# Performance work log

Measured on AMD Instinct MI355X. Metric: run time of the kernel, lower is better.

The kernel has to match this reference:

```python
import jax, jax.numpy as jnp
import numpy as np

N_NODES = 50000
N_EDGES = 800000
IN_C = 128
HID = 128
OUT_C = 64
N_GRAPHS = 256


def setup_inputs() -> dict:
    key = jax.random.key(0)
    ks = jax.random.split(key, 12)
    x = jax.random.normal(ks[0], (N_NODES, IN_C), dtype=jnp.float32)
    edge_index = jax.random.randint(ks[1], (2, N_EDGES), 0, N_NODES, dtype=jnp.int32)
    batch = jnp.sort(jax.random.randint(ks[2], (N_NODES,), 0, N_GRAPHS, dtype=jnp.int32))
    def lin(k, fan_in, fan_out):
        bound = 1.0 / np.sqrt(fan_in)
        kw, kb = jax.random.split(k)
        W = jax.random.uniform(kw, (fan_in, fan_out), minval=-bound, maxval=bound, dtype=jnp.float32)
        b = jax.random.uniform(kb, (fan_out,), minval=-bound, maxval=bound, dtype=jnp.float32)
        return W, b
    W1a, b1a = lin(ks[3], IN_C, HID)
    W1b, b1b = lin(ks[4], HID, HID)
    W2a, b2a = lin(ks[5], HID, HID)
    W2b, b2b = lin(ks[6], HID, HID)
    Wl, bl = lin(ks[7], HID, OUT_C)
    return {"x": x, "edge_index": edge_index, "batch": batch,
            "W1a": W1a, "b1a": b1a, "W1b": W1b, "b1b": b1b,
            "W2a": W2a, "b2a": b2a, "W2b": W2b, "b2b": b2b,
            "Wl": Wl, "bl": bl}


def gin_conv(x, edge_index, Wa, ba, Wb, bb):
    # GINConv with eps=0: h_i = MLP(x_i + sum_{j->i} x_j)
    src, dst = edge_index[0], edge_index[1]
    agg = jax.ops.segment_sum(x[src], dst, num_segments=x.shape[0])  # [N, d]
    h = x + agg
    h = jax.nn.relu(h @ Wa + ba) @ Wb + bb
    return h


def reference(x, edge_index, batch, W1a, b1a, W1b, b1b, W2a, b2a, W2b, b2b, Wl, bl):
    h = gin_conv(x, edge_index, W1a, b1a, W1b, b1b)
    h = gin_conv(h, edge_index, W2a, b2a, W2b, b2b)
    # global mean pool over graphs in the batch
    sums = jax.ops.segment_sum(h, batch, num_segments=N_GRAPHS)          # [G, HID]
    cnts = jax.ops.segment_sum(jnp.ones((h.shape[0],), h.dtype), batch, num_segments=N_GRAPHS)
    pooled = sums / jnp.maximum(cnts, 1.0)[:, None]
    return pooled @ Wl + bl  # [G, OUT_C]
```

## Files before the change

### kernel.cpp

```cpp
#include <hip/hip_runtime.h>

constexpr int N  = 50000;
constexpr int E  = 800000;
constexpr int C  = 128;
constexpr int G  = 256;
constexpr int OC = 64;
constexpr int D  = 64;

constexpr int NBUCK = 196;
constexpr int BCAP  = 5120;
constexpr int EPB = 2048;
constexpr int EB = (E + EPB - 1) / EPB;
constexpr int WB = 256;
constexpr int XB = (N * C / 8 + 255) / 256;
constexpr int GB = (N + 255) / 256;

typedef __attribute__((ext_vector_type(8))) short short8;
typedef __attribute__((ext_vector_type(4))) float f32x4;
typedef __attribute__((ext_vector_type(2))) float f32x2;

__device__ __forceinline__ unsigned int au(float f) { return __float_as_uint(f); }

__device__ __forceinline__ unsigned short f2bf(float f) {
    unsigned int u = au(f);
    u += 0x7fffu + ((u >> 16) & 1u);
    return (unsigned short)(u >> 16);
}
__device__ __forceinline__ unsigned int pack_bf16(float lo, float hi) {
    return ((au(hi) + 0x8000u) & 0xFFFF0000u) | ((au(lo) + 0x8000u) >> 16);
}

__device__ __forceinline__ void acc16(f32x2* a, uint4 v) {
    a[0] += __builtin_amdgcn_cvt_pk_f32_fp8((int)v.x, false);
    a[1] += __builtin_amdgcn_cvt_pk_f32_fp8((int)v.x, true);
    a[2] += __builtin_amdgcn_cvt_pk_f32_fp8((int)v.y, false);
    a[3] += __builtin_amdgcn_cvt_pk_f32_fp8((int)v.y, true);
    a[4] += __builtin_amdgcn_cvt_pk_f32_fp8((int)v.z, false);
    a[5] += __builtin_amdgcn_cvt_pk_f32_fp8((int)v.z, true);
    a[6] += __builtin_amdgcn_cvt_pk_f32_fp8((int)v.w, false);
    a[7] += __builtin_amdgcn_cvt_pk_f32_fp8((int)v.w, true);
}
__device__ __forceinline__ void set16(f32x2* a, uint4 v) {
    a[0] = __builtin_amdgcn_cvt_pk_f32_fp8((int)v.x, false);
    a[1] = __builtin_amdgcn_cvt_pk_f32_fp8((int)v.x, true);
    a[2] = __builtin_amdgcn_cvt_pk_f32_fp8((int)v.y, false);
    a[3] = __builtin_amdgcn_cvt_pk_f32_fp8((int)v.y, true);
    a[4] = __builtin_amdgcn_cvt_pk_f32_fp8((int)v.z, false);
    a[5] = __builtin_amdgcn_cvt_pk_f32_fp8((int)v.z, true);
    a[6] = __builtin_amdgcn_cvt_pk_f32_fp8((int)v.w, false);
    a[7] = __builtin_amdgcn_cvt_pk_f32_fp8((int)v.w, true);
}


__global__ __launch_bounds__(256) void build_prep_kernel(const int* __restrict__ src,
                                                         const int* __restrict__ dst,
                                                         int* __restrict__ bcount,
                                                         unsigned int* __restrict__ bucketbuf,
                                                         const float* __restrict__ W1a,
                                                         const float* __restrict__ W1b,
                                                         const float* __restrict__ W2a,
                                                         const float* __restrict__ W2b,
                                                         const float* __restrict__ x,
                                                         unsigned short* __restrict__ wt,
                                                         unsigned int* __restrict__ x8,
                                                         const int* __restrict__ batch,
                                                         int* __restrict__ gcnt) {
    int b = blockIdx.x;
    if (b < EB) {
        __shared__ int lcount[NBUCK];
        __shared__ int lbase[NBUCK];
        __shared__ int lcur[NBUCK];
        int tid = threadIdx.x;
        for (int i = tid; i < NBUCK; i += 256) { lcount[i] = 0; lcur[i] = 0; }
        __syncthreads();
        int e0 = b * EPB;
        int sv[8], dv[8];
#pragma unroll
        for (int i = 0; i < 8; ++i) {
            int e = e0 + i * 256 + tid;
            if (e < E) {
                sv[i] = src[e];
                dv[i] = dst[e];
                atomicAdd(&lcount[dv[i] >> 8], 1);
            } else {
                dv[i] = -1;
            }
        }
        __syncthreads();
        if (tid < NBUCK) {
            int c = lcount[tid];
            lbase[tid] = (c > 0) ? atomicAdd(&bcount[tid], c) : 0;
        }
        __syncthreads();
#pragma unroll
        for (int i = 0; i < 8; ++i) {
            if (dv[i] >= 0) {
                int bk = dv[i] >> 8;
                int pos = lbase[bk] + atomicAdd(&lcur[bk], 1);
                if (pos < BCAP)
                    bucketbuf[(size_t)bk * BCAP + pos] =
                        ((unsigned int)sv[i] << 16) | (unsigned int)(dv[i] & 255);
            }
        }
    } else if (b < EB + WB) {
        const float* Ws[4] = {W1a, W1b, W2a, W2b};
        int idx = (b - EB) * 256 + threadIdx.x;
        int which = idx >> 14;
        int el    = idx & 16383;
        int n = el >> 7, k = el & 127;
        wt[idx] = f2bf(Ws[which][k * 128 + n]);
    } else if (b < EB + WB + XB) {
        int idx = (b - EB - WB) * 256 + threadIdx.x;
        const float4* x4 = (const float4*)x;
        float4 v0 = x4[idx * 2];
        float4 v1 = x4[idx * 2 + 1];
        unsigned int lo = 0, hi = 0;
        lo = (unsigned int)__builtin_amdgcn_cvt_pk_fp8_f32(v0.x, v0.y, (int)lo, false);
        lo = (unsigned int)__builtin_amdgcn_cvt_pk_fp8_f32(v0.z, v0.w, (int)lo, true);
        hi = (unsigned int)__builtin_amdgcn_cvt_pk_fp8_f32(v1.x, v1.y, (int)hi, false);
        hi = (unsigned int)__builtin_amdgcn_cvt_pk_fp8_f32(v1.z, v1.w, (int)hi, true);
        ((uint2*)x8)[idx] = make_uint2(lo, hi);
    } else {
        __shared__ int h[G];
        int tid = threadIdx.x;
        h[tid] = 0;
        __syncthreads();
        int i = (b - EB - WB - XB) * 256 + tid;
        if (i < N) atomicAdd(&h[batch[i]], 1);
        __syncthreads();
        int c = h[tid];
        if (c > 0) atomicAdd(&gcnt[tid], c);
    }
}


__global__ __launch_bounds__(256) void bucket_fill_kernel(const int* __restrict__ bcount,
                                                          const unsigned int* __restrict__ bucketbuf,
                                                          unsigned short* __restrict__ ell,
                                                          int* __restrict__ deg) {
    __shared__ int lcur[256];
    int b = blockIdx.x;
    int tid = threadIdx.x;
    lcur[tid] = 0;
    __syncthreads();
    int cnt = min(bcount[b], BCAP);
    const unsigned int* buf = bucketbuf + (size_t)b * BCAP;
    int nbase = b << 8;
    for (int i = tid; i < cnt; i += 256) {
        unsigned int e = buf[i];
        int dlow = (int)(e & 255u);
        int p = atomicAdd(&lcur[dlow], 1);
        if (p < D) ell[(size_t)(nbase + dlow) * D + p] = (unsigned short)(e >> 16);
    }
    __syncthreads();
    int node = nbase + tid;
    if (node < N) deg[node] = lcur[tid];
}


__global__ __launch_bounds__(512, 6) void conv_kernel(const unsigned char* __restrict__ Fg,
                                                      const int* __restrict__ deg,
                                                      const unsigned short* __restrict__ ell,
                                                      const unsigned short* __restrict__ WaT,
                                                      const float* __restrict__ ba,
                                                      const unsigned short* __restrict__ WbT,
                                                      const float* __restrict__ bb,
                                                      unsigned char* __restrict__ Hg8,
                                                      const int* __restrict__ batch,
                                                      float* __restrict__ gsum,
                                                      int outFp8) {
    constexpr int LD = 136;
    __shared__ short Xl[64 * LD];
    __shared__ short Wl[128 * LD];
    int tid  = threadIdx.x;
    int lane = tid & 63;
    int wave = tid >> 6;
    int row0 = blockIdx.x * 64;

    const short8* Wa8 = (const short8*)WaT;
#pragma unroll
    for (int i = tid; i < 2048; i += 512) {
        int r = i >> 4, c = i & 15;
        *((short8*)(Wl + r * LD) + c) = Wa8[i];
    }

    {
        int grp = tid >> 3;
        int l   = tid & 7;
        const uint4* F16 = (const uint4*)Fg;
        int n = row0 + grp;
        f32x2 a[8];
        if (n < N) {
            int dg = min(deg[n], D);
            const uint4* irow = (const uint4*)(ell + (size_t)n * D);
            set16(a, F16[(size_t)n * 8 + l]);
            int nb  = dg >> 3;
            int rem = dg & 7;
            if (nb > 0) {
                uint4 i4 = irow[0];
                int t0 = (int)(i4.x & 0xffffu), t1 = (int)(i4.x >> 16);
                int t2 = (int)(i4.y & 0xffffu), t3 = (int)(i4.y >> 16);
                int t4 = (int)(i4.z & 0xffffu), t5 = (int)(i4.z >> 16);
                int t6 = (int)(i4.w & 0xffffu), t7 = (int)(i4.w >> 16);
                uint4 v0 = F16[(size_t)t0 * 8 + l];
                uint4 v1 = F16[(size_t)t1 * 8 + l];
                uint4 v2 = F16[(size_t)t2 * 8 + l];
                uint4 v3 = F16[(size_t)t3 * 8 + l];
                uint4 v4 = F16[(size_t)t4 * 8 + l];
                uint4 v5 = F16[(size_t)t5 * 8 + l];
                uint4 v6 = F16[(size_t)t6 * 8 + l];
                uint4 v7 = F16[(size_t)t7 * 8 + l];
                for (int b = 1; b < nb; ++b) {
                    uint4 j4 = irow[b];
                    int u0 = (int)(j4.x & 0xffffu), u1 = (int)(j4.x >> 16);
                    int u2 = (int)(j4.y & 0xffffu), u3 = (int)(j4.y >> 16);
                    int u4 = (int)(j4.z & 0xffffu), u5 = (int)(j4.z >> 16);
                    int u6 = (int)(j4.w & 0xffffu), u7 = (int)(j4.w >> 16);
                    uint4 w0 = F16[(size_t)u0 * 8 + l];
                    uint4 w1 = F16[(size_t)u1 * 8 + l];
                    uint4 w2 = F16[(size_t)u2 * 8 + l];
                    uint4 w3 = F16[(size_t)u3 * 8 + l];
                    uint4 w4 = F16[(size_t)u4 * 8 + l];
                    uint4 w5 = F16[(size_t)u5 * 8 + l];
                    uint4 w6 = F16[(size_t)u6 * 8 + l];
                    uint4 w7 = F16[(size_t)u7 * 8 + l];
                    acc16(a, v0); acc16(a, v1); acc16(a, v2); acc16(a, v3);
                    acc16(a, v4); acc16(a, v5); acc16(a, v6); acc16(a, v7);
                    v0 = w0; v1 = w1; v2 = w2; v3 = w3;
                    v4 = w4; v5 = w5; v6 = w6; v7 = w7;
                }
                acc16(a, v0); acc16(a, v1); acc16(a, v2); acc16(a, v3);
                acc16(a, v4); acc16(a, v5); acc16(a, v6); acc16(a, v7);
            }
            if (rem) {
                uint4 i4 = irow[nb];
                int t0 = (int)(i4.x & 0xffffu), t1 = (int)(i4.x >> 16);
                int t2 = (int)(i4.y & 0xffffu), t3 = (int)(i4.y >> 16);
                int t4 = (int)(i4.z & 0xffffu), t5 = (int)(i4.z >> 16);
                int t6 = (int)(i4.w & 0xffffu), t7 = (int)(i4.w >> 16);
                int tv[8] = {t0, t1, t2, t3, t4, t5, t6, t7};
#pragma unroll
                for (int m = 0; m < 7; ++m) {
                    if (m < rem) {
                        uint4 v = F16[(size_t)tv[m] * 8 + l];
                        acc16(a, v);
                    }
                }
            }
        } else {
#pragma unroll
            for (int q = 0; q < 8; ++q) a[q] = (f32x2){0.f, 0.f};
        }
        uint4 o0, o1;
        o0.x = pack_bf16(a[0].x, a[0].y); o0.y = pack_bf16(a[1].x, a[1].y);
        o0.z = pack_bf16(a[2].x, a[2].y); o0.w = pack_bf16(a[3].x, a[3].y);
        o1.x = pack_bf16(a[4].x, a[4].y); o1.y = pack_bf16(a[5].x, a[5].y);
        o1.z = pack_bf16(a[6].x, a[6].y); o1.w = pack_bf16(a[7].x, a[7].y);
        uint4* xp = (uint4*)(Xl + grp * LD + l * 16);
        xp[0] = o0;
        xp[1] = o1;
    }

    int mw = wave >> 2, nw = wave & 3;
    int lid = lane & 15, quad = lane >> 4;

    f32x4 acc[2][2];
#pragma unroll
    for (int nt = 0; nt < 2; ++nt) {
        float b = ba[nw * 32 + nt * 16 + lid];
        acc[0][nt] = (f32x4){b, b, b, b};
        acc[1][nt] = (f32x4){b, b, b, b};
    }
    __syncthreads();

#pragma unroll
    for (int ks = 0; ks < 4; ++ks) {
        short8 a0 = *(const short8*)(Xl + (mw * 32 + lid) * LD + ks * 32 + quad * 8);
        short8 a1 = *(const short8*)(Xl + (mw * 32 + 16 + lid) * LD + ks * 32 + quad * 8);
#pragma unroll
        for (int nt = 0; nt < 2; ++nt) {
            short8 bf = *(const short8*)(Wl + (nw * 32 + nt * 16 + lid) * LD + ks * 32 + quad * 8);
            acc[0][nt] = __builtin_amdgcn_mfma_f32_16x16x32_bf16(a0, bf, acc[0][nt], 0, 0, 0);
            acc[1][nt] = __builtin_amdgcn_mfma_f32_16x16x32_bf16(a1, bf, acc[1][nt], 0, 0, 0);
        }
    }
    __syncthreads();

#pragma unroll
    for (int mt = 0; mt < 2; ++mt) {
#pragma unroll
        for (int nt = 0; nt < 2; ++nt) {
            int mbase = mw * 32 + mt * 16 + quad * 4;
            int n = nw * 32 + nt * 16 + lid;
            f32x4 v = acc[mt][nt];
#pragma unroll
            for (int r = 0; r < 4; ++r)
                Xl[(mbase + r) * LD + n] = (short)f2bf(fmaxf(v[r], 0.f));
        }
    }
    const short8* Wb8 = (const short8*)WbT;
#pragma unroll
    for (int i = tid; i < 2048; i += 512) {
        int r = i >> 4, c = i & 15;
        *((short8*)(Wl + r * LD) + c) = Wb8[i];
    }
    f32x4 acc2[2][2];
#pragma unroll
    for (int nt = 0; nt < 2; ++nt) {
        float b = bb[nw * 32 + nt * 16 + lid];
        acc2[0][nt] = (f32x4){b, b, b, b};
        acc2[1][nt] = (f32x4){b, b, b, b};
    }
    __syncthreads();

#pragma unroll
    for (int ks = 0; ks < 4; ++ks) {
        short8 a0 = *(const short8*)(Xl + (mw * 32 + lid) * LD + ks * 32 + quad * 8);
        short8 a1 = *(const short8*)(Xl + (mw * 32 + 16 + lid) * LD + ks * 32 + quad * 8);
#pragma unroll
        for (int nt = 0; nt < 2; ++nt) {
            short8 bf = *(const short8*)(Wl + (nw * 32 + nt * 16 + lid) * LD + ks * 32 + quad * 8);
            acc2[0][nt] = __builtin_amdgcn_mfma_f32_16x16x32_bf16(a0, bf, acc2[0][nt], 0, 0, 0);
            acc2[1][nt] = __builtin_amdgcn_mfma_f32_16x16x32_bf16(a1, bf, acc2[1][nt], 0, 0, 0);
        }
    }

#pragma unroll
    for (int mt = 0; mt < 2; ++mt) {
#pragma unroll
        for (int nt = 0; nt < 2; ++nt) {
            int mbase = row0 + mw * 32 + mt * 16 + quad * 4;
            int n = nw * 32 + nt * 16 + lid;
            f32x4 v = acc2[mt][nt];
            if (outFp8) {
#pragma unroll
                for (int r = 0; r < 4; ++r) {
                    int row = mbase + r;
                    if (row < N) {
                        unsigned int p = (unsigned int)__builtin_amdgcn_cvt_pk_fp8_f32(v[r], 0.f, 0, false);
                        Hg8[(size_t)row * 128 + n] = (unsigned char)(p & 0xFF);
                    }
                }
            } else {
                int gprev = -1;
                float s = 0.f;
#pragma unroll
                for (int r = 0; r < 4; ++r) {
                    int row = mbase + r;
                    if (row < N) {
                        int g = batch[row];
                        if (g != gprev) {
                            if (gprev >= 0) atomicAdd(&gsum[gprev * C + n], s);
                            gprev = g;
                            s = 0.f;
                        }
                        s += v[r];
                    }
                }
                if (gprev >= 0) atomicAdd(&gsum[gprev * C + n], s);
            }
        }
    }
}


__global__ __launch_bounds__(64) void head_kernel(const float* __restrict__ gsum,
                                                  const int* __restrict__ gcnt,
                                                  const float* __restrict__ Wl,
                                                  const float* __restrict__ bl,
                                                  float* __restrict__ out) {
    int g = blockIdx.x;
    int t = threadIdx.x;
    __shared__ float pooled[C];
    float inv = 1.0f / (float)max(gcnt[g], 1);
    pooled[t]      = gsum[g * C + t] * inv;
    pooled[t + 64] = gsum[g * C + 64 + t] * inv;
    __syncthreads();
    float o = bl[t];
#pragma unroll 4
    for (int k = 0; k < C; ++k) o += pooled[k] * Wl[k * OC + t];
    out[g * OC + t] = o;
}


extern "C" void kernel_launch(void* const* d_in, const int* in_sizes, int n_in,
                              void* d_out, int out_size, void* d_ws, size_t ws_size,
                              hipStream_t stream) {
    const float* x    = (const float*)d_in[0];
    const int*   ei   = (const int*)d_in[1];
    const int*   bat  = (const int*)d_in[2];
    const float* W1a  = (const float*)d_in[3];
    const float* b1a  = (const float*)d_in[4];
    const float* W1b  = (const float*)d_in[5];
    const float* b1b  = (const float*)d_in[6];
    const float* W2a  = (const float*)d_in[7];
    const float* b2a  = (const float*)d_in[8];
    const float* W2b  = (const float*)d_in[9];
    const float* b2b  = (const float*)d_in[10];
    const float* Wl   = (const float*)d_in[11];
    const float* bl   = (const float*)d_in[12];
    float*       out  = (float*)d_out;

    float* gsum    = (float*)d_ws;
    int*   gcnt    = (int*)(gsum + G * C);
    int*   bcount  = gcnt + G;
    int*   deg     = bcount + NBUCK;
    unsigned int* bucketbuf = (unsigned int*)(deg + N);
    unsigned short* ell = (unsigned short*)(bucketbuf + (size_t)NBUCK * BCAP);
    unsigned short* wt  = ell + (size_t)N * D;
    unsigned char*  x8  = (unsigned char*)(wt + 4 * 16384);
    unsigned char*  h8  = x8 + (size_t)N * 128;

    const unsigned short* wt1a = wt;
    const unsigned short* wt1b = wt + 16384;
    const unsigned short* wt2a = wt + 2 * 16384;
    const unsigned short* wt2b = wt + 3 * 16384;

    const int* src = ei;
    const int* dst = ei + E;

    hipMemsetAsync(gsum, 0, (size_t)(G * C + G + NBUCK) * sizeof(int), stream);

    build_prep_kernel<<<EB + WB + XB + GB, 256, 0, stream>>>(src, dst, bcount, bucketbuf,
                                                             W1a, W1b, W2a, W2b, x,
                                                             wt, (unsigned int*)x8,
                                                             bat, gcnt);
    bucket_fill_kernel<<<NBUCK, 256, 0, stream>>>(bcount, bucketbuf, ell, deg);

    int mb = (N + 63) / 64;

    conv_kernel<<<mb, 512, 0, stream>>>(x8, deg, ell, wt1a, b1a, wt1b, b1b,
                                        h8, nullptr, nullptr, 1);
    conv_kernel<<<mb, 512, 0, stream>>>(h8, deg, ell, wt2a, b2a, wt2b, b2b,
                                        nullptr, bat, gsum, 0);

    head_kernel<<<G, 64, 0, stream>>>(gsum, gcnt, Wl, bl, out);
}
```

Baseline: 214.2 us.

## Build ELL adjacency directly with global atomics, drop bucket pass

Replaces the two-stage bucketed CSR/ELL build (local bucket counting plus a separate bucket_fill kernel) with a single pass that does a global atomicAdd on each destination's degree and writes the source index straight into the ELL slot. This removes one kernel launch and the intermediate bucket buffer traffic, and the memset grows to zero the degree array. It also lowers the conv_kernel occupancy hint in launch_bounds from 6 to 4, which allows more registers per thread. The trade-off is 800k scattered global atomics on random nodes instead of mostly shared-memory atomics.

```diff
diff --git a/kernel.cpp b/kernel.cpp
--- a/kernel.cpp
+++ b/kernel.cpp
@@ -7,8 +7,6 @@
 constexpr int OC = 64;
 constexpr int D  = 64;
 
-constexpr int NBUCK = 196;
-constexpr int BCAP  = 5120;
 constexpr int EPB = 2048;
 constexpr int EB = (E + EPB - 1) / EPB;
 constexpr int WB = 256;
@@ -54,8 +52,8 @@
 
 __global__ __launch_bounds__(256) void build_prep_kernel(const int* __restrict__ src,
                                                          const int* __restrict__ dst,
-                                                         int* __restrict__ bcount,
-                                                         unsigned int* __restrict__ bucketbuf,
+                                                         int* __restrict__ deg,
+                                                         unsigned short* __restrict__ ell,
                                                          const float* __restrict__ W1a,
                                                          const float* __restrict__ W1b,
                                                          const float* __restrict__ W2a,
@@ -67,39 +65,16 @@
                                                          int* __restrict__ gcnt) {
     int b = blockIdx.x;
     if (b < EB) {
-        __shared__ int lcount[NBUCK];
-        __shared__ int lbase[NBUCK];
-        __shared__ int lcur[NBUCK];
+        int e0 = b * EPB;
         int tid = threadIdx.x;
-        for (int i = tid; i < NBUCK; i += 256) { lcount[i] = 0; lcur[i] = 0; }
-        __syncthreads();
-        int e0 = b * EPB;
-        int sv[8], dv[8];
 #pragma unroll
         for (int i = 0; i < 8; ++i) {
             int e = e0 + i * 256 + tid;
             if (e < E) {
-                sv[i] = src[e];
-                dv[i] = dst[e];
-                atomicAdd(&lcount[dv[i] >> 8], 1);
-            } else {
-                dv[i] = -1;
-            }
-        }
-        __syncthreads();
-        if (tid < NBUCK) {
-            int c = lcount[tid];
-            lbase[tid] = (c > 0) ? atomicAdd(&bcount[tid], c) : 0;
-        }
-        __syncthreads();
-#pragma unroll
-        for (int i = 0; i < 8; ++i) {
-            if (dv[i] >= 0) {
-                int bk = dv[i] >> 8;
-                int pos = lbase[bk] + atomicAdd(&lcur[bk], 1);
-                if (pos < BCAP)
-                    bucketbuf[(size_t)bk * BCAP + pos] =
-                        ((unsigned int)sv[i] << 16) | (unsigned int)(dv[i] & 255);
+                int s = src[e];
+                int d = dst[e];
+                int p = atomicAdd(&deg[d], 1);
+                if (p < D) ell[(size_t)d * D + p] = (unsigned short)s;
             }
         }
     } else if (b < EB + WB) {
@@ -134,31 +109,7 @@
 }
 
 
-__global__ __launch_bounds__(256) void bucket_fill_kernel(const int* __restrict__ bcount,
-                                                          const unsigned int* __restrict__ bucketbuf,
-                                                          unsigned short* __restrict__ ell,
-                                                          int* __restrict__ deg) {
-    __shared__ int lcur[256];
-    int b = blockIdx.x;
-    int tid = threadIdx.x;
-    lcur[tid] = 0;
-    __syncthreads();
-    int cnt = min(bcount[b], BCAP);
-    const unsigned int* buf = bucketbuf + (size_t)b * BCAP;
-    int nbase = b << 8;
-    for (int i = tid; i < cnt; i += 256) {
-        unsigned int e = buf[i];
-        int dlow = (int)(e & 255u);
-        int p = atomicAdd(&lcur[dlow], 1);
-        if (p < D) ell[(size_t)(nbase + dlow) * D + p] = (unsigned short)(e >> 16);
-    }
-    __syncthreads();
-    int node = nbase + tid;
-    if (node < N) deg[node] = lcur[tid];
-}
-
-
-__global__ __launch_bounds__(512, 6) void conv_kernel(const unsigned char* __restrict__ Fg,
+__global__ __launch_bounds__(512, 4) void conv_kernel(const unsigned char* __restrict__ Fg,
                                                       const int* __restrict__ deg,
                                                       const unsigned short* __restrict__ ell,
                                                       const unsigned short* __restrict__ WaT,
@@ -403,10 +354,8 @@
 
     float* gsum    = (float*)d_ws;
     int*   gcnt    = (int*)(gsum + G * C);
-    int*   bcount  = gcnt + G;
-    int*   deg     = bcount + NBUCK;
-    unsigned int* bucketbuf = (unsigned int*)(deg + N);
-    unsigned short* ell = (unsigned short*)(bucketbuf + (size_t)NBUCK * BCAP);
+    int*   deg     = gcnt + G;
+    unsigned short* ell = (unsigned short*)(deg + N);
     unsigned short* wt  = ell + (size_t)N * D;
     unsigned char*  x8  = (unsigned char*)(wt + 4 * 16384);
     unsigned char*  h8  = x8 + (size_t)N * 128;
@@ -419,13 +368,12 @@
     const int* src = ei;
     const int* dst = ei + E;
 
-    hipMemsetAsync(gsum, 0, (size_t)(G * C + G + NBUCK) * sizeof(int), stream);
-
-    build_prep_kernel<<<EB + WB + XB + GB, 256, 0, stream>>>(src, dst, bcount, bucketbuf,
+    hipMemsetAsync(gsum, 0, (size_t)(G * C + G + N) * sizeof(int), stream);
+
+    build_prep_kernel<<<EB + WB + XB + GB, 256, 0, stream>>>(src, dst, deg, ell,
                                                              W1a, W1b, W2a, W2b, x,
                                                              wt, (unsigned int*)x8,
                                                              bat, gcnt);
-    bucket_fill_kernel<<<NBUCK, 256, 0, stream>>>(bcount, bucketbuf, ell, deg);
 
     int mb = (N + 63) / 64;
 
```

Result: slower. 233.8 us (+9.2%).

## Reassociate GIN linear layers: transform before aggregation and fold consecutive weights

Applied to the files above, without the earlier changes.

Uses linearity of aggregation to apply W1a before the neighbor sum, folds W1b·W2a into a single precomputed matrix (and bias b1b into a degree-scaled term), and folds W2b into the head weights so the last conv needs only aggregation, ReLU and pooling. This removes two of the four per-node GEMMs and the x fp8 conversion pass. In exchange it adds a separate dense GEMM kernel before aggregation and quantizes pre-activation products to fp8, which changes numerics. The gather loop is also reduced from 8-wide to 4-wide index batches.

```diff
diff --git a/kernel.cpp b/kernel.cpp
--- a/kernel.cpp
+++ b/kernel.cpp
@@ -10,10 +10,11 @@
 constexpr int NBUCK = 196;
 constexpr int BCAP  = 5120;
 constexpr int EPB = 2048;
-constexpr int EB = (E + EPB - 1) / EPB;
-constexpr int WB = 256;
-constexpr int XB = (N * C / 8 + 255) / 256;
-constexpr int GB = (N + 255) / 256;
+constexpr int EB  = (E + EPB - 1) / EPB;
+constexpr int WB1 = 64;
+constexpr int WXB = 64;
+constexpr int WHB = 32;
+constexpr int GB  = (N + 255) / 256;
 
 typedef __attribute__((ext_vector_type(8))) short short8;
 typedef __attribute__((ext_vector_type(4))) float f32x4;
@@ -51,6 +52,44 @@
     a[7] = __builtin_amdgcn_cvt_pk_f32_fp8((int)v.w, true);
 }
 
+__device__ __forceinline__ void gather_rows(f32x2* a, const uint4* F16,
+                                            const unsigned short* irow, int dg, int l) {
+    const uint2* i2 = (const uint2*)irow;
+    int nb  = dg >> 2;
+    int rem = dg & 3;
+    if (nb > 0) {
+        uint2 iu = i2[0];
+        int t0 = (int)(iu.x & 0xffffu), t1 = (int)(iu.x >> 16);
+        int t2 = (int)(iu.y & 0xffffu), t3 = (int)(iu.y >> 16);
+        uint4 v0 = F16[(size_t)t0 * 8 + l];
+        uint4 v1 = F16[(size_t)t1 * 8 + l];
+        uint4 v2 = F16[(size_t)t2 * 8 + l];
+        uint4 v3 = F16[(size_t)t3 * 8 + l];
+        for (int b = 1; b < nb; ++b) {
+            uint2 ju = i2[b];
+            int u0 = (int)(ju.x & 0xffffu), u1 = (int)(ju.x >> 16);
+            int u2 = (int)(ju.y & 0xffffu), u3 = (int)(ju.y >> 16);
+            uint4 w0 = F16[(size_t)u0 * 8 + l];
+            uint4 w1 = F16[(size_t)u1 * 8 + l];
+            uint4 w2 = F16[(size_t)u2 * 8 + l];
+            uint4 w3 = F16[(size_t)u3 * 8 + l];
+            acc16(a, v0); acc16(a, v1); acc16(a, v2); acc16(a, v3);
+            v0 = w0; v1 = w1; v2 = w2; v3 = w3;
+        }
+        acc16(a, v0); acc16(a, v1); acc16(a, v2); acc16(a, v3);
+    }
+    if (rem) {
+        const unsigned short* ir = irow + nb * 4;
+#pragma unroll
+        for (int m = 0; m < 3; ++m) {
+            if (m < rem) {
+                uint4 v = F16[(size_t)ir[m] * 8 + l];
+                acc16(a, v);
+            }
+        }
+    }
+}
+
 
 __global__ __launch_bounds__(256) void build_prep_kernel(const int* __restrict__ src,
                                                          const int* __restrict__ dst,
@@ -60,17 +99,23 @@
                                                          const float* __restrict__ W1b,
                                                          const float* __restrict__ W2a,
                                                          const float* __restrict__ W2b,
-                                                         const float* __restrict__ x,
-                                                         unsigned short* __restrict__ wt,
-                                                         unsigned int* __restrict__ x8,
+                                                         const float* __restrict__ Wl,
+                                                         const float* __restrict__ bl,
+                                                         const float* __restrict__ b1b,
+                                                         const float* __restrict__ b2b,
+                                                         unsigned short* __restrict__ wt1a,
+                                                         unsigned short* __restrict__ wtx,
+                                                         float* __restrict__ Whead,
+                                                         float* __restrict__ c1,
+                                                         float* __restrict__ bhead,
                                                          const int* __restrict__ batch,
                                                          int* __restrict__ gcnt) {
     int b = blockIdx.x;
+    int tid = threadIdx.x;
     if (b < EB) {
         __shared__ int lcount[NBUCK];
         __shared__ int lbase[NBUCK];
         __shared__ int lcur[NBUCK];
-        int tid = threadIdx.x;
         for (int i = tid; i < NBUCK; i += 256) { lcount[i] = 0; lcur[i] = 0; }
         __syncthreads();
         int e0 = b * EPB;
@@ -102,30 +147,38 @@
                         ((unsigned int)sv[i] << 16) | (unsigned int)(dv[i] & 255);
             }
         }
-    } else if (b < EB + WB) {
-        const float* Ws[4] = {W1a, W1b, W2a, W2b};
-        int idx = (b - EB) * 256 + threadIdx.x;
-        int which = idx >> 14;
-        int el    = idx & 16383;
-        int n = el >> 7, k = el & 127;
-        wt[idx] = f2bf(Ws[which][k * 128 + n]);
-    } else if (b < EB + WB + XB) {
-        int idx = (b - EB - WB) * 256 + threadIdx.x;
-        const float4* x4 = (const float4*)x;
-        float4 v0 = x4[idx * 2];
-        float4 v1 = x4[idx * 2 + 1];
-        unsigned int lo = 0, hi = 0;
-        lo = (unsigned int)__builtin_amdgcn_cvt_pk_fp8_f32(v0.x, v0.y, (int)lo, false);
-        lo = (unsigned int)__builtin_amdgcn_cvt_pk_fp8_f32(v0.z, v0.w, (int)lo, true);
-        hi = (unsigned int)__builtin_amdgcn_cvt_pk_fp8_f32(v1.x, v1.y, (int)hi, false);
-        hi = (unsigned int)__builtin_amdgcn_cvt_pk_fp8_f32(v1.z, v1.w, (int)hi, true);
-        ((uint2*)x8)[idx] = make_uint2(lo, hi);
+    } else if (b < EB + WB1) {
+        int idx = (b - EB) * 256 + tid;
+        int n = idx >> 7, k = idx & 127;
+        wt1a[idx] = f2bf(W1a[k * 128 + n]);
+    } else if (b < EB + WB1 + WXB) {
+        int idx = (b - EB - WB1) * 256 + tid;
+        int i = idx >> 7, j = idx & 127;
+        float acc = 0.f;
+        for (int k = 0; k < 128; ++k) acc += W1b[i * 128 + k] * W2a[k * 128 + j];
+        wtx[j * 128 + i] = f2bf(acc);
+    } else if (b < EB + WB1 + WXB + WHB) {
+        int idx = (b - EB - WB1 - WXB) * 256 + tid;
+        int i = idx >> 6, j = idx & 63;
+        float acc = 0.f;
+        for (int k = 0; k < 128; ++k) acc += W2b[i * 128 + k] * Wl[k * OC + j];
+        Whead[i * OC + j] = acc;
+    } else if (b == EB + WB1 + WXB + WHB) {
+        if (tid < 128) {
+            float acc = 0.f;
+            for (int k = 0; k < 128; ++k) acc += b1b[k] * W2a[k * 128 + tid];
+            c1[tid] = acc;
+        } else if (tid < 192) {
+            int j = tid - 128;
+            float acc = bl[j];
+            for (int k = 0; k < 128; ++k) acc += b2b[k] * Wl[k * OC + j];
+            bhead[j] = acc;
+        }
     } else {
         __shared__ int h[G];
-        int tid = threadIdx.x;
         h[tid] = 0;
         __syncthreads();
-        int i = (b - EB - WB - XB) * 256 + tid;
+        int i = (b - (EB + WB1 + WXB + WHB + 1)) * 256 + tid;
         if (i < N) atomicAdd(&h[batch[i]], 1);
         __syncthreads();
         int c = h[tid];
@@ -158,94 +211,111 @@
 }
 
 
-__global__ __launch_bounds__(512, 6) void conv_kernel(const unsigned char* __restrict__ Fg,
-                                                      const int* __restrict__ deg,
-                                                      const unsigned short* __restrict__ ell,
-                                                      const unsigned short* __restrict__ WaT,
-                                                      const float* __restrict__ ba,
-                                                      const unsigned short* __restrict__ WbT,
-                                                      const float* __restrict__ bb,
-                                                      unsigned char* __restrict__ Hg8,
-                                                      const int* __restrict__ batch,
-                                                      float* __restrict__ gsum,
-                                                      int outFp8) {
+__global__ __launch_bounds__(256, 4) void gemma_kernel(const float* __restrict__ x,
+                                                       const unsigned short* __restrict__ wt1a,
+                                                       unsigned char* __restrict__ z1) {
     constexpr int LD = 136;
     __shared__ short Xl[64 * LD];
     __shared__ short Wl[128 * LD];
-    int tid  = threadIdx.x;
-    int lane = tid & 63;
-    int wave = tid >> 6;
+    int tid = threadIdx.x;
+    int lane = tid & 63, wave = tid >> 6;
     int row0 = blockIdx.x * 64;
 
-    const short8* Wa8 = (const short8*)WaT;
+    const short8* Wg = (const short8*)wt1a;
+#pragma unroll
+    for (int i = tid; i < 2048; i += 256) {
+        int r = i >> 4, c = i & 15;
+        *((short8*)(Wl + r * LD) + c) = Wg[i];
+    }
+    const float4* x4 = (const float4*)(x + (size_t)row0 * C);
+#pragma unroll
+    for (int i = tid; i < 2048; i += 256) {
+        int r = i >> 5, c4 = i & 31;
+        float4 v = (row0 + r < N) ? x4[i] : make_float4(0.f, 0.f, 0.f, 0.f);
+        uint2 u;
+        u.x = pack_bf16(v.x, v.y);
+        u.y = pack_bf16(v.z, v.w);
+        *(uint2*)(Xl + r * LD + c4 * 4) = u;
+    }
+
+    int mw = wave >> 1, nw = wave & 1;
+    int lid = lane & 15, quad = lane >> 4;
+    f32x4 acc[2][4];
+#pragma unroll
+    for (int nt = 0; nt < 4; ++nt) {
+        acc[0][nt] = (f32x4){0.f, 0.f, 0.f, 0.f};
+        acc[1][nt] = (f32x4){0.f, 0.f, 0.f, 0.f};
+    }
+    __syncthreads();
+
+#pragma unroll
+    for (int ks = 0; ks < 4; ++ks) {
+        short8 a0 = *(const short8*)(Xl + (mw * 32 + lid) * LD + ks * 32 + quad * 8);
+        short8 a1 = *(const short8*)(Xl + (mw * 32 + 16 + lid) * LD + ks * 32 + quad * 8);
+#pragma unroll
+        for (int nt = 0; nt < 4; ++nt) {
+            short8 bf = *(const short8*)(Wl + (nw * 64 + nt * 16 + lid) * LD + ks * 32 + quad * 8);
+            acc[0][nt] = __builtin_amdgcn_mfma_f32_16x16x32_bf16(a0, bf, acc[0][nt], 0, 0, 0);
+            acc[1][nt] = __builtin_amdgcn_mfma_f32_16x16x32_bf16(a1, bf, acc[1][nt], 0, 0, 0);
+        }
+    }
+
+#pragma unroll
+    for (int mt = 0; mt < 2; ++mt) {
+#pragma unroll
+        for (int nt = 0; nt < 4; ++nt) {
+            int mbase = row0 + mw * 32 + mt * 16 + quad * 4;
+            int n = nw * 64 + nt * 16 + lid;
+            f32x4 v = acc[mt][nt];
+#pragma unroll
+            for (int r = 0; r < 4; ++r) {
+                int row = mbase + r;
+                if (row < N) {
+                    unsigned int p = (unsigned int)__builtin_amdgcn_cvt_pk_fp8_f32(v[r], 0.f, 0, false);
+                    z1[(size_t)row * 128 + n] = (unsigned char)(p & 0xFF);
+                }
+            }
+        }
+    }
+}
+
+
+__global__ __launch_bounds__(512, 6) void k2_kernel(const unsigned char* __restrict__ z1,
+                                                    const int* __restrict__ deg,
+                                                    const unsigned short* __restrict__ ell,
+                                                    const unsigned short* __restrict__ wtx,
+                                                    const float* __restrict__ b1a,
+                                                    unsigned char* __restrict__ z2) {
+    constexpr int LD = 136;
+    __shared__ short Xl[64 * LD];
+    __shared__ short Wl[128 * LD];
+    int tid = threadIdx.x;
+    int lane = tid & 63, wave = tid >> 6;
+    int row0 = blockIdx.x * 64;
+
+    const short8* Wg = (const short8*)wtx;
 #pragma unroll
     for (int i = tid; i < 2048; i += 512) {
         int r = i >> 4, c = i & 15;
-        *((short8*)(Wl + r * LD) + c) = Wa8[i];
+        *((short8*)(Wl + r * LD) + c) = Wg[i];
     }
 
     {
         int grp = tid >> 3;
         int l   = tid & 7;
-        const uint4* F16 = (const uint4*)Fg;
+        const uint4* F16 = (const uint4*)z1;
         int n = row0 + grp;
         f32x2 a[8];
         if (n < N) {
-            int dg = min(deg[n], D);
-            const uint4* irow = (const uint4*)(ell + (size_t)n * D);
+            int dgc = min(deg[n], D);
             set16(a, F16[(size_t)n * 8 + l]);
-            int nb  = dg >> 3;
-            int rem = dg & 7;
-            if (nb > 0) {
-                uint4 i4 = irow[0];
-                int t0 = (int)(i4.x & 0xffffu), t1 = (int)(i4.x >> 16);
-                int t2 = (int)(i4.y & 0xffffu), t3 = (int)(i4.y >> 16);
-                int t4 = (int)(i4.z & 0xffffu), t5 = (int)(i4.z >> 16);
-                int t6 = (int)(i4.w & 0xffffu), t7 = (int)(i4.w >> 16);
-                uint4 v0 = F16[(size_t)t0 * 8 + l];
-                uint4 v1 = F16[(size_t)t1 * 8 + l];
-                uint4 v2 = F16[(size_t)t2 * 8 + l];
-                uint4 v3 = F16[(size_t)t3 * 8 + l];
-                uint4 v4 = F16[(size_t)t4 * 8 + l];
-                uint4 v5 = F16[(size_t)t5 * 8 + l];
-                uint4 v6 = F16[(size_t)t6 * 8 + l];
-                uint4 v7 = F16[(size_t)t7 * 8 + l];
-                for (int b = 1; b < nb; ++b) {
-                    uint4 j4 = irow[b];
-                    int u0 = (int)(j4.x & 0xffffu), u1 = (int)(j4.x >> 16);
-                    int u2 = (int)(j4.y & 0xffffu), u3 = (int)(j4.y >> 16);
-                    int u4 = (int)(j4.z & 0xffffu), u5 = (int)(j4.z >> 16);
-                    int u6 = (int)(j4.w & 0xffffu), u7 = (int)(j4.w >> 16);
-                    uint4 w0 = F16[(size_t)u0 * 8 + l];
-                    uint4 w1 = F16[(size_t)u1 * 8 + l];
-                    uint4 w2 = F16[(size_t)u2 * 8 + l];
-                    uint4 w3 = F16[(size_t)u3 * 8 + l];
-                    uint4 w4 = F16[(size_t)u4 * 8 + l];
-                    uint4 w5 = F16[(size_t)u5 * 8 + l];
-                    uint4 w6 = F16[(size_t)u6 * 8 + l];
-                    uint4 w7 = F16[(size_t)u7 * 8 + l];
-                    acc16(a, v0); acc16(a, v1); acc16(a, v2); acc16(a, v3);
-                    acc16(a, v4); acc16(a, v5); acc16(a, v6); acc16(a, v7);
-                    v0 = w0; v1 = w1; v2 = w2; v3 = w3;
-                    v4 = w4; v5 = w5; v6 = w6; v7 = w7;
-                }
-                acc16(a, v0); acc16(a, v1); acc16(a, v2); acc16(a, v3);
-                acc16(a, v4); acc16(a, v5); acc16(a, v6); acc16(a, v7);
-            }
-            if (rem) {
-                uint4 i4 = irow[nb];
-                int t0 = (int)(i4.x & 0xffffu), t1 = (int)(i4.x >> 16);
-                int t2 = (int)(i4.y & 0xffffu), t3 = (int)(i4.y >> 16);
-                int t4 = (int)(i4.z & 0xffffu), t5 = (int)(i4.z >> 16);
-                int t6 = (int)(i4.w & 0xffffu), t7 = (int)(i4.w >> 16);
-                int tv[8] = {t0, t1, t2, t3, t4, t5, t6, t7};
-#pragma unroll
-                for (int m = 0; m < 7; ++m) {
-                    if (m < rem) {
-                        uint4 v = F16[(size_t)tv[m] * 8 + l];
-                        acc16(a, v);
-                    }
-                }
+            gather_rows(a, F16, ell + (size_t)n * D, dgc, l);
+            const f32x2* bp = (const f32x2*)(b1a + l * 16);
+#pragma unroll
+            for (int q = 0; q < 8; ++q) {
+                a[q] += bp[q];
+                a[q].x = fmaxf(a[q].x, 0.f);
+                a[q].y = fmaxf(a[q].y, 0.f);
             }
         } else {
 #pragma unroll
@@ -263,13 +333,11 @@
 
     int mw = wave >> 2, nw = wave & 3;
     int lid = lane & 15, quad = lane >> 4;
-
     f32x4 acc[2][2];
 #pragma unroll
     for (int nt = 0; nt < 2; ++nt) {
-        float b = ba[nw * 32 + nt * 16 + lid];
-        acc[0][nt] = (f32x4){b, b, b, b};
-        acc[1][nt] = (f32x4){b, b, b, b};
+        acc[0][nt] = (f32x4){0.f, 0.f, 0.f, 0.f};
+        acc[1][nt] = (f32x4){0.f, 0.f, 0.f, 0.f};
     }
     __syncthreads();
 
@@ -284,46 +352,6 @@
             acc[1][nt] = __builtin_amdgcn_mfma_f32_16x16x32_bf16(a1, bf, acc[1][nt], 0, 0, 0);
         }
     }
-    __syncthreads();
-
-#pragma unroll
-    for (int mt = 0; mt < 2; ++mt) {
-#pragma unroll
-        for (int nt = 0; nt < 2; ++nt) {
-            int mbase = mw * 32 + mt * 16 + quad * 4;
-            int n = nw * 32 + nt * 16 + lid;
-            f32x4 v = acc[mt][nt];
-#pragma unroll
-            for (int r = 0; r < 4; ++r)
-                Xl[(mbase + r) * LD + n] = (short)f2bf(fmaxf(v[r], 0.f));
-        }
-    }
-    const short8* Wb8 = (const short8*)WbT;
-#pragma unroll
-    for (int i = tid; i < 2048; i += 512) {
-        int r = i >> 4, c = i & 15;
-        *((short8*)(Wl + r * LD) + c) = Wb8[i];
-    }
-    f32x4 acc2[2][2];
-#pragma unroll
-    for (int nt = 0; nt < 2; ++nt) {
-        float b = bb[nw * 32 + nt * 16 + lid];
-        acc2[0][nt] = (f32x4){b, b, b, b};
-        acc2[1][nt] = (f32x4){b, b, b, b};
-    }
-    __syncthreads();
-
-#pragma unroll
-    for (int ks = 0; ks < 4; ++ks) {
-        short8 a0 = *(const short8*)(Xl + (mw * 32 + lid) * LD + ks * 32 + quad * 8);
-        short8 a1 = *(const short8*)(Xl + (mw * 32 + 16 + lid) * LD + ks * 32 + quad * 8);
-#pragma unroll
-        for (int nt = 0; nt < 2; ++nt) {
-            short8 bf = *(const short8*)(Wl + (nw * 32 + nt * 16 + lid) * LD + ks * 32 + quad * 8);
-            acc2[0][nt] = __builtin_amdgcn_mfma_f32_16x16x32_bf16(a0, bf, acc2[0][nt], 0, 0, 0);
-            acc2[1][nt] = __builtin_amdgcn_mfma_f32_16x16x32_bf16(a1, bf, acc2[1][nt], 0, 0, 0);
-        }
-    }
 
 #pragma unroll
     for (int mt = 0; mt < 2; ++mt) {
@@ -331,43 +359,97 @@
         for (int nt = 0; nt < 2; ++nt) {
             int mbase = row0 + mw * 32 + mt * 16 + quad * 4;
             int n = nw * 32 + nt * 16 + lid;
-            f32x4 v = acc2[mt][nt];
-            if (outFp8) {
-#pragma unroll
-                for (int r = 0; r < 4; ++r) {
-                    int row = mbase + r;
-                    if (row < N) {
-                        unsigned int p = (unsigned int)__builtin_amdgcn_cvt_pk_fp8_f32(v[r], 0.f, 0, false);
-                        Hg8[(size_t)row * 128 + n] = (unsigned char)(p & 0xFF);
-                    }
+            f32x4 v = acc[mt][nt];
+#pragma unroll
+            for (int r = 0; r < 4; ++r) {
+                int row = mbase + r;
+                if (row < N) {
+                    unsigned int p = (unsigned int)__builtin_amdgcn_cvt_pk_fp8_f32(v[r], 0.f, 0, false);
+                    z2[(size_t)row * 128 + n] = (unsigned char)(p & 0xFF);
                 }
-            } else {
-                int gprev = -1;
-                float s = 0.f;
-#pragma unroll
-                for (int r = 0; r < 4; ++r) {
-                    int row = mbase + r;
-                    if (row < N) {
-                        int g = batch[row];
-                        if (g != gprev) {
-                            if (gprev >= 0) atomicAdd(&gsum[gprev * C + n], s);
-                            gprev = g;
-                            s = 0.f;
-                        }
-                        s += v[r];
-                    }
-                }
-                if (gprev >= 0) atomicAdd(&gsum[gprev * C + n], s);
-            }
-        }
+            }
+        }
+    }
+}
+
+
+__global__ __launch_bounds__(512, 6) void k3_kernel(const unsigned char* __restrict__ z2,
+                                                    const int* __restrict__ deg,
+                                                    const unsigned short* __restrict__ ell,
+                                                    const float* __restrict__ c1,
+                                                    const float* __restrict__ b2a,
+                                                    const int* __restrict__ batch,
+                                                    float* __restrict__ gsum) {
+    constexpr int LD = 136;
+    __shared__ short Xl[64 * LD];
+    int tid = threadIdx.x;
+    int lane = tid & 63, wave = tid >> 6;
+    int row0 = blockIdx.x * 64;
+
+    {
+        int grp = tid >> 3;
+        int l   = tid & 7;
+        const uint4* F16 = (const uint4*)z2;
+        int n = row0 + grp;
+        f32x2 a[8];
+        if (n < N) {
+            int dfull = deg[n];
+            int dgc = min(dfull, D);
+            set16(a, F16[(size_t)n * 8 + l]);
+            gather_rows(a, F16, ell + (size_t)n * D, dgc, l);
+            float degf = (float)(1 + dfull);
+            const f32x2* c1p = (const f32x2*)(c1 + l * 16);
+            const f32x2* b2p = (const f32x2*)(b2a + l * 16);
+#pragma unroll
+            for (int q = 0; q < 8; ++q) {
+                a[q] += degf * c1p[q] + b2p[q];
+                a[q].x = fmaxf(a[q].x, 0.f);
+                a[q].y = fmaxf(a[q].y, 0.f);
+            }
+        } else {
+#pragma unroll
+            for (int q = 0; q < 8; ++q) a[q] = (f32x2){0.f, 0.f};
+        }
+        uint4 o0, o1;
+        o0.x = pack_bf16(a[0].x, a[0].y); o0.y = pack_bf16(a[1].x, a[1].y);
+        o0.z = pack_bf16(a[2].x, a[2].y); o0.w = pack_bf16(a[3].x, a[3].y);
+        o1.x = pack_bf16(a[4].x, a[4].y); o1.y = pack_bf16(a[5].x, a[5].y);
+        o1.z = pack_bf16(a[6].x, a[6].y); o1.w = pack_bf16(a[7].x, a[7].y);
+        uint4* xp = (uint4*)(Xl + grp * LD + l * 16);
+        xp[0] = o0;
+        xp[1] = o1;
+    }
+    __syncthreads();
+
+    int r0 = wave * 8;
+    int gprev = -1;
+    float a0 = 0.f, a1 = 0.f;
+    for (int rr = 0; rr < 8; ++rr) {
+        int row = row0 + r0 + rr;
+        if (row >= N) break;
+        int g = batch[row];
+        if (g != gprev) {
+            if (gprev >= 0) {
+                atomicAdd(&gsum[gprev * C + 2 * lane], a0);
+                atomicAdd(&gsum[gprev * C + 2 * lane + 1], a1);
+            }
+            gprev = g; a0 = 0.f; a1 = 0.f;
+        }
+        unsigned int pv = *(const unsigned int*)(Xl + (r0 + rr) * LD + 2 * lane);
+        a0 += __uint_as_float((pv & 0xffffu) << 16);
+        a1 += __uint_as_float(pv & 0xffff0000u);
+    }
+    if (gprev >= 0) {
+        atomicAdd(&gsum[gprev * C + 2 * lane], a0);
+        atomicAdd(&gsum[gprev * C + 2 * lane + 1], a1);
     }
 }
 
 
 __global__ __launch_bounds__(64) void head_kernel(const float* __restrict__ gsum,
                                                   const int* __restrict__ gcnt,
-                                                  const float* __restrict__ Wl,
-                                                  const float* __restrict__ bl,
+                                                  const float* __restrict__ Whead,
+                                                  const float* __restrict__ bhead,
                                                   float* __restrict__ out) {
     int g = blockIdx.x;
     int t = threadIdx.x;
@@ -376,9 +458,9 @@
     pooled[t]      = gsum[g * C + t] * inv;
     pooled[t + 64] = gsum[g * C + 64 + t] * inv;
     __syncthreads();
-    float o = bl[t];
+    float o = bhead[t];
 #pragma unroll 4
-    for (int k = 0; k < C; ++k) o += pooled[k] * Wl[k * OC + t];
+    for (int k = 0; k < C; ++k) o += pooled[k] * Whead[k * OC + t];
     out[g * OC + t] = o;
 }
 
@@ -405,34 +487,31 @@
     int*   gcnt    = (int*)(gsum + G * C);
     int*   bcount  = gcnt + G;
     int*   deg     = bcount + NBUCK;
-    unsigned int* bucketbuf = (unsigned int*)(deg + N);
-    unsigned short* ell = (unsigned short*)(bucketbuf + (size_t)NBUCK * BCAP);
-    unsigned short* wt  = ell + (size_t)N * D;
-    unsigned char*  x8  = (unsigned char*)(wt + 4 * 16384);
-    unsigned char*  h8  = x8 + (size_t)N * 128;
-
-    const unsigned short* wt1a = wt;
-    const unsigned short* wt1b = wt + 16384;
-    const unsigned short* wt2a = wt + 2 * 16384;
-    const unsigned short* wt2b = wt + 3 * 16384;
+    unsigned int*   bucketbuf = (unsigned int*)(deg + N);
+    unsigned short* ell  = (unsigned short*)(bucketbuf + (size_t)NBUCK * BCAP);
+    unsigned short* wt1a = ell + (size_t)N * D;
+    unsigned short* wtx  = wt1a + 16384;
+    float* Whead = (float*)(wtx + 16384);
+    float* c1    = Whead + 128 * OC;
+    float* bhead = c1 + 128;
+    unsigned char* z1 = (unsigned char*)(bhead + OC);
+    unsigned char* z2 = z1 + (size_t)N * 128;
 
     const int* src = ei;
     const int* dst = ei + E;
 
     hipMemsetAsync(gsum, 0, (size_t)(G * C + G + NBUCK) * sizeof(int), stream);
 
-    build_prep_kernel<<<EB + WB + XB + GB, 256, 0, stream>>>(src, dst, bcount, bucketbuf,
-                                                             W1a, W1b, W2a, W2b, x,
-                                                             wt, (unsigned int*)x8,
-                                                             bat, gcnt);
+    build_prep_kernel<<<EB + WB1 + WXB + WHB + 1 + GB, 256, 0, stream>>>(
+        src, dst, bcount, bucketbuf, W1a, W1b, W2a, W2b, Wl, bl, b1b, b2b,
+        wt1a, wtx, Whead, c1, bhead, bat, gcnt);
+
     bucket_fill_kernel<<<NBUCK, 256, 0, stream>>>(bcount, bucketbuf, ell, deg);
 
     int mb = (N + 63) / 64;
 
-    conv_kernel<<<mb, 512, 0, stream>>>(x8, deg, ell, wt1a, b1a, wt1b, b1b,
-                                        h8, nullptr, nullptr, 1);
-    conv_kernel<<<mb, 512, 0, stream>>>(h8, deg, ell, wt2a, b2a, wt2b, b2b,
-                                        nullptr, bat, gsum, 0);
-
-    head_kernel<<<G, 64, 0, stream>>>(gsum, gcnt, Wl, bl, out);
-}
+    gemma_kernel<<<mb, 256, 0, stream>>>(x, wt1a, z1);
+    k2_kernel<<<mb, 512, 0, stream>>>(z1, deg, ell, wtx, b1a, z2);
+    k3_kernel<<<mb, 512, 0, stream>>>(z2, deg, ell, c1, b2a, bat, gsum);
+    head_kernel<<<G, 64, 0, stream>>>(gsum, gcnt, Whead, bhead, out);
+}
```

Measured after the change: 197.1 us. 8.0% less time.
